# Optimization experiments

Measured on AMD Instinct MI355X. Metric: run time of the kernel, lower is better.

## Reference

```python
import jax, jax.numpy as jnp
import numpy as np
import math

N = 50000      # nodes per type
E = 800000     # edges per relation
IN = 256
OUT = 256
H = 8
DK = OUT // H  # 32
SQRT_DK = math.sqrt(DK)


def setup_inputs() -> dict:
    key = jax.random.key(0)
    ks = jax.random.split(key, 24)
    s = 0.02
    inp = {
        'h_A': jax.random.normal(ks[0], (N, IN), jnp.float32),
        'h_B': jax.random.normal(ks[1], (N, IN), jnp.float32),
        'src0': jax.random.randint(ks[2], (E,), 0, N, jnp.int32),
        'dst0': jax.random.randint(ks[3], (E,), 0, N, jnp.int32),
        'src1': jax.random.randint(ks[4], (E,), 0, N, jnp.int32),
        'dst1': jax.random.randint(ks[5], (E,), 0, N, jnp.int32),
        'src2': jax.random.randint(ks[6], (E,), 0, N, jnp.int32),
        'dst2': jax.random.randint(ks[7], (E,), 0, N, jnp.int32),
        # per-node-type linears (2 types): y = x @ W + b
        'Wk': jax.random.normal(ks[8], (2, IN, OUT), jnp.float32) * s,
        'bk': jnp.zeros((2, OUT), jnp.float32),
        'Wq': jax.random.normal(ks[9], (2, IN, OUT), jnp.float32) * s,
        'bq': jnp.zeros((2, OUT), jnp.float32),
        'Wv': jax.random.normal(ks[10], (2, IN, OUT), jnp.float32) * s,
        'bv': jnp.zeros((2, OUT), jnp.float32),
        'Wa': jax.random.normal(ks[11], (2, OUT, OUT), jnp.float32) * s,
        'ba': jnp.zeros((2, OUT), jnp.float32),
        # per-relation params (3 relations)
        'rel_att': jax.random.normal(ks[12], (3, H, DK, DK), jnp.float32) * (1.0 / math.sqrt(DK)),
        'rel_msg': jax.random.normal(ks[13], (3, H, DK, DK), jnp.float32) * (1.0 / math.sqrt(DK)),
        'rel_pri': jnp.ones((3, H), jnp.float32),
        'skip': jnp.ones((2,), jnp.float32),
    }
    return inp


def _relation_flow(k_src, v_src, q_dst, A_r, M_r, pri_r, src, dst):
    # k_src/v_src/q_dst: [N,H,DK] ; A_r,M_r: [H,DK,DK] ; pri_r: [H]
    k = jnp.einsum('bij,ijk->bik', k_src, A_r)
    v = jnp.einsum('bij,ijk->bik', v_src, M_r)
    # edge-wise dot: sum_d q[dst] * k[src] per head -> [E,H]
    score = jnp.einsum('ehd,ehd->eh', q_dst[dst], k[src]) * pri_r / SQRT_DK
    # edge softmax normalized by dst
    mx = jax.ops.segment_max(score, dst, num_segments=N)
    ex = jnp.exp(score - mx[dst])
    den = jax.ops.segment_sum(ex, dst, num_segments=N)
    attn = ex / den[dst]                       # [E,H]
    msg = v[src] * attn[:, :, None]            # [E,H,DK]
    return jax.ops.segment_sum(msg, dst, num_segments=N)  # [N,H,DK]


def reference(h_A, h_B, src0, dst0, src1, dst1, src2, dst2,
              Wk, bk, Wq, bq, Wv, bv, Wa, ba,
              rel_att, rel_msg, rel_pri, skip):
    h = [h_A, h_B]
    hd = lambda x: x.reshape(-1, H, DK)
    k = [hd(h[t] @ Wk[t] + bk[t]) for t in range(2)]
    q = [hd(h[t] @ Wq[t] + bq[t]) for t in range(2)]
    v = [hd(h[t] @ Wv[t] + bv[t]) for t in range(2)]

    # relations: r0: A->B, r1: B->A, r2: A->B
    t0 = _relation_flow(k[0], v[0], q[1], rel_att[0], rel_msg[0], rel_pri[0], src0, dst0)
    t1 = _relation_flow(k[1], v[1], q[0], rel_att[1], rel_msg[1], rel_pri[1], src1, dst1)
    t2 = _relation_flow(k[0], v[0], q[1], rel_att[2], rel_msg[2], rel_pri[2], src2, dst2)

    # cross_reducer='mean' over relations delivering to each dst type
    t_A = t1.reshape(N, OUT)
    t_B = ((t0 + t2) * 0.5).reshape(N, OUT)

    def out_for(tn, nid):
        alpha = jax.nn.sigmoid(skip[nid])
        trans = tn @ Wa[nid] + ba[nid]   # dropout is identity at eval
        return trans * alpha + h[nid] * (1.0 - alpha)

    new_h_A = out_for(t_A, 0)
    new_h_B = out_for(t_B, 1)
    return jnp.stack([new_h_A, new_h_B])  # [2, N, OUT]
```

## Files before the change

kernel.cpp:

```cpp
#include <hip/hip_runtime.h>
#include <math.h>

#define NN 50000
#define EE 800000
#define CC 256
#define NS (NN * CC)
#define NBK 782
#define BCAP 2048
#define P1T 2048
#define NT1 391

typedef __attribute__((ext_vector_type(4))) float f32x4;
typedef __attribute__((ext_vector_type(8))) short bf16x8;
typedef __attribute__((ext_vector_type(4))) unsigned int u32x4;
typedef __attribute__((ext_vector_type(2))) unsigned int u32x2;

__device__ __forceinline__ float bf2f(unsigned int u) {
    union { unsigned int i; float f; } c; c.i = u << 16; return c.f;
}
__device__ __forceinline__ unsigned short f2bf(float f) {
    union { float f; unsigned int i; } c; c.f = f;
    unsigned int u = c.i;
    u += 0x7fffu + ((u >> 16) & 1u);
    return (unsigned short)(u >> 16);
}

#if __has_builtin(__builtin_amdgcn_cvt_f32_fp8) && __has_builtin(__builtin_amdgcn_cvt_pk_fp8_f32)
#define HW_FP8 1
#else
#define HW_FP8 0
#endif

__device__ __forceinline__ unsigned char sw_f2fp8(float f) {
    float a = fabsf(f);
    unsigned s = (f < 0.f) ? 0x80u : 0u;
    if (a >= 448.f) return (unsigned char)(s | 0x7Eu);
    if (a < 0.015625f) {
        int q = (int)(a * 512.f + 0.5f);
        return (unsigned char)(s | (unsigned)q);
    }
    int e = (int)floorf(log2f(a));
    float m = ldexpf(a, -e);
    int q = (int)(m * 8.f + 0.5f);
    if (q == 16) { q = 8; e += 1; }
    if (e > 8) return (unsigned char)(s | 0x7Eu);
    return (unsigned char)(s | ((unsigned)(e + 7) << 3) | (unsigned)(q - 8));
}
__device__ __forceinline__ float sw_fp82f(unsigned b) {
    unsigned s = (b & 0x80u) << 24;
    unsigned exp = (b >> 3) & 0xFu, man = b & 7u;
    float val = (exp == 0) ? ldexpf((float)man, -9)
                           : ldexpf((float)(8u | man), (int)exp - 10);
    unsigned r = __builtin_bit_cast(unsigned, val) | s;
    return __builtin_bit_cast(float, r);
}
__device__ __forceinline__ unsigned char f2fp8(float f) {
#if HW_FP8
    return (unsigned char)(__builtin_amdgcn_cvt_pk_fp8_f32(f, 0.f, 0, false) & 0xff);
#else
    return sw_f2fp8(f);
#endif
}

__global__ void tobf_kernel(const float* __restrict__ hA, const float* __restrict__ hB,
                            unsigned short* __restrict__ h_bf)
{
    int id = blockIdx.x * 256 + threadIdx.x;
    if (id >= 2 * NS / 8) return;
    size_t base = (size_t)id * 8;
    const float* src = (base < (size_t)NS) ? (hA + base) : (hB + (base - NS));
    f32x4 a = *(const f32x4*)src;
    f32x4 b = *(const f32x4*)(src + 4);
    u32x4 o;
    o[0] = (unsigned)f2bf(a[0]) | ((unsigned)f2bf(a[1]) << 16);
    o[1] = (unsigned)f2bf(a[2]) | ((unsigned)f2bf(a[3]) << 16);
    o[2] = (unsigned)f2bf(b[0]) | ((unsigned)f2bf(b[1]) << 16);
    o[3] = (unsigned)f2bf(b[2]) | ((unsigned)f2bf(b[3]) << 16);
    *(u32x4*)(h_bf + base) = o;
}

__global__ void setup_kernel(const float* __restrict__ Wk, const float* __restrict__ bk,
                             const float* __restrict__ Wq, const float* __restrict__ bq,
                             const float* __restrict__ Wv, const float* __restrict__ bv,
                             const float* __restrict__ Wa,
                             const float* __restrict__ rel_att, const float* __restrict__ rel_msg,
                             unsigned short* __restrict__ WT, float* __restrict__ ball,
                             const int* __restrict__ d0, const int* __restrict__ d1,
                             const int* __restrict__ d2, int* __restrict__ bcnt)
{
    int b = blockIdx.x;
    const int ts[3] = {0, 1, 0};
    if (b >= 2568) {
        int bb = b - 2568;
        int r = bb / NT1, tile = bb - r * NT1;
        const int* dp = r == 0 ? d0 : (r == 1 ? d1 : d2);
        __shared__ int hist[NBK];
        for (int i = threadIdx.x; i < NBK; i += 256) hist[i] = 0;
        __syncthreads();
        int base = tile * P1T;
        int lim = base + P1T; if (lim > EE) lim = EE;
        for (int i = base + threadIdx.x; i < lim; i += 256)
            atomicAdd(&hist[dp[i] >> 6], 1);
        __syncthreads();
        for (int i = threadIdx.x; i < NBK; i += 256)
            if (hist[i]) atomicAdd(&bcnt[r * NBK + i], hist[i]);
        return;
    }
    int id = b * 256 + threadIdx.x;
    if (id < 2 * 65536) {
        int t = id >> 16, rem = id & 65535;
        int n = rem >> 8, k = rem & 255;
        WT[t * 65536 + n * 256 + k] = f2bf(Wq[t * 65536 + k * 256 + n]);
    } else if (id < 5 * 65536) {
        int id2 = id - 2 * 65536;
        int r = id2 >> 16, rem = id2 & 65535;
        int n = rem >> 8, k = rem & 255;
        int h = n >> 5, j = n & 31;
        const float* wkb = Wk + ts[r] * 65536 + k * 256 + h * 32;
        const float* ab  = rel_att + r * 8192 + h * 1024 + j;
        float s = 0.f;
        #pragma unroll 8
        for (int d = 0; d < 32; ++d) s += wkb[d] * ab[d * 32];
        WT[(2 + r) * 65536 + n * 256 + k] = f2bf(s);
    } else if (id < 8 * 65536) {
        int id2 = id - 5 * 65536;
        int r = id2 >> 16, rem = id2 & 65535;
        int n = rem >> 8, k = rem & 255;
        int h = n >> 5, j = n & 31;
        const float* wvb = Wv + ts[r] * 65536 + k * 256 + h * 32;
        const float* mb  = rel_msg + r * 8192 + h * 1024 + j;
        float s = 0.f;
        #pragma unroll 8
        for (int d = 0; d < 32; ++d) s += wvb[d] * mb[d * 32];
        WT[(5 + r) * 65536 + n * 256 + k] = f2bf(s);
    } else if (id < 10 * 65536) {
        int id2 = id - 8 * 65536;
        int t = id2 >> 16, rem = id2 & 65535;
        int n = rem >> 8, k = rem & 255;
        WT[(8 + t) * 65536 + n * 256 + k] = f2bf(Wa[t * 65536 + k * 256 + n]);
    } else if (id < 10 * 65536 + 2048) {
        int id2 = id - 10 * 65536;
        int z = id2 >> 8, c = id2 & 255;
        float v;
        if (z < 2) {
            v = bq[z * 256 + c];
        } else if (z < 5) {
            int r = z - 2, h = c >> 5, j = c & 31;
            const float* bkb = bk + ts[r] * 256 + h * 32;
            const float* ab  = rel_att + r * 8192 + h * 1024 + j;
            v = 0.f;
            for (int d = 0; d < 32; ++d) v += bkb[d] * ab[d * 32];
        } else {
            int r = z - 5, h = c >> 5, j = c & 31;
            const float* bvb = bv + ts[r] * 256 + h * 32;
            const float* mb  = rel_msg + r * 8192 + h * 1024 + j;
            v = 0.f;
            for (int d = 0; d < 32; ++d) v += bvb[d] * mb[d * 32];
        }
        ball[z * 256 + c] = v;
    }
}

__global__ __launch_bounds__(1024) void bscan_kernel(const int* __restrict__ bcnt,
                                                     int* __restrict__ bbase,
                                                     int* __restrict__ bcur)
{
    int r = blockIdx.x;
    int t = threadIdx.x, lane = t & 63, w = t >> 6;
    __shared__ int wsum[16];
    int x = (t < NBK) ? bcnt[r * NBK + t] : 0;
    int v = x;
    #pragma unroll
    for (int ofs = 1; ofs < 64; ofs <<= 1) {
        int y = __shfl_up(v, ofs);
        if (lane >= ofs) v += y;
    }
    if (lane == 63) wsum[w] = v;
    __syncthreads();
    if (t < 16) {
        int wv = wsum[t];
        #pragma unroll
        for (int ofs = 1; ofs < 16; ofs <<= 1) {
            int y = __shfl_up(wv, ofs);
            if (t >= ofs) wv += y;
        }
        wsum[t] = wv;
    }
    __syncthreads();
    int excl = (w > 0 ? wsum[w - 1] : 0) + v - x;
    if (t < NBK) { bbase[r * (NBK + 1) + t] = excl; bcur[r * NBK + t] = excl; }
    if (t == NBK - 1) bbase[r * (NBK + 1) + NBK] = excl + x;
}

__global__ __launch_bounds__(256) void p1_kernel(const int* __restrict__ s0, const int* __restrict__ s1,
                                                 const int* __restrict__ s2,
                                                 const int* __restrict__ d0, const int* __restrict__ d1,
                                                 const int* __restrict__ d2,
                                                 int* __restrict__ bcur, unsigned int* __restrict__ srcS)
{
    int bb = blockIdx.x;
    int r = bb / NT1, tile = bb - r * NT1;
    const int* sp = r == 0 ? s0 : (r == 1 ? s1 : s2);
    const int* dp = r == 0 ? d0 : (r == 1 ? d1 : d2);
    __shared__ int hist[NBK];
    __shared__ int lbase[NBK];
    for (int i = threadIdx.x; i < NBK; i += 256) hist[i] = 0;
    __syncthreads();
    int base = tile * P1T;
    int lim = base + P1T; if (lim > EE) lim = EE;
    for (int i = base + threadIdx.x; i < lim; i += 256)
        atomicAdd(&hist[dp[i] >> 6], 1);
    __syncthreads();
    for (int i = threadIdx.x; i < NBK; i += 256)
        lbase[i] = hist[i] ? atomicAdd(&bcur[r * NBK + i], hist[i]) : 0;
    __syncthreads();
    unsigned int* out = srcS + (size_t)r * EE;
    for (int i = base + threadIdx.x; i < lim; i += 256) {
        int dv = dp[i];
        int bk = dv >> 6;
        int pos = atomicAdd(&lbase[bk], 1);
        out[pos] = ((unsigned)sp[i] << 6) | (unsigned)(dv & 63);
    }
}

__global__ __launch_bounds__(256) void p2_kernel(const int* __restrict__ bbase,
                                                 unsigned int* __restrict__ srcS,
                                                 int* __restrict__ offs)
{
    int r = blockIdx.x / NBK, bk = blockIdx.x - r * NBK;
    int base = bbase[r * (NBK + 1) + bk];
    int n = bbase[r * (NBK + 1) + bk + 1] - base;
    unsigned int* seg = srcS + (size_t)r * EE + base;
    __shared__ unsigned int vals[BCAP];
    __shared__ unsigned int sorted[BCAP];
    __shared__ int hist[64], hcur[64];
    int t = threadIdx.x;
    if (t < 64) hist[t] = 0;
    __syncthreads();
    for (int i = t; i < n; i += 256) {
        unsigned int v = seg[i];
        vals[i] = v;
        atomicAdd(&hist[v & 63], 1);
    }
    __syncthreads();
    if (t < 64) {
        int x = hist[t], v = x;
        #pragma unroll
        for (int ofs = 1; ofs < 64; ofs <<= 1) {
            int y = __shfl_up(v, ofs);
            if (t >= ofs) v += y;
        }
        int excl = v - x;
        hcur[t] = excl;
        int d = bk * 64 + t;
        if (d < NN) offs[r * (NN + 1) + d] = base + excl;
    }
    if (bk == NBK - 1 && t == 64) offs[r * (NN + 1) + NN] = EE;
    __syncthreads();
    for (int i = t; i < n; i += 256) {
        unsigned int v = vals[i];
        int pos = atomicAdd(&hcur[v & 63], 1);
        sorted[pos] = v >> 6;
    }
    __syncthreads();
    for (int i = t; i < n; i += 256) seg[i] = sorted[i];
}

__device__ __forceinline__ void gemm_body(const unsigned short* __restrict__ A,
                                          const unsigned short* __restrict__ W,
                                          const float* __restrict__ bias,
                                          unsigned short* __restrict__ Obf,
                                          unsigned char* __restrict__ Of8,
                                          int mBase, int nBase)
{
    __shared__ __align__(16) unsigned short As[128 * 64];
    __shared__ __align__(16) unsigned short Bs[128 * 64];

    int tid = threadIdx.x;
    int lane = tid & 63, wid = tid >> 6;
    int warpM = wid >> 1, warpN = wid & 1;

    f32x4 acc[4][4];
    #pragma unroll
    for (int i = 0; i < 4; ++i)
        #pragma unroll
        for (int j = 0; j < 4; ++j) acc[i][j] = (f32x4){0.f, 0.f, 0.f, 0.f};

    for (int kt = 0; kt < 4; ++kt) {
        int k0 = kt * 64;
        __syncthreads();
        #pragma unroll
        for (int i = 0; i < 4; ++i) {
            int c = tid + i * 256;
            int row = c >> 3, cc = c & 7;
            int gr = mBase + row; if (gr > NN - 1) gr = NN - 1;
            u32x4 av = *(const u32x4*)(A + (size_t)gr * CC + k0 + cc * 8);
            int sb = row * 128 + ((cc * 16) ^ ((row & 7) << 4));
            *(u32x4*)((char*)As + sb) = av;
            u32x4 bv = *(const u32x4*)(W + (nBase + row) * 256 + k0 + cc * 8);
            *(u32x4*)((char*)Bs + sb) = bv;
        }
        __syncthreads();
        #pragma unroll
        for (int kk = 0; kk < 2; ++kk) {
            bf16x8 af[4], bfr[4];
            int kb = kk * 64 + (lane >> 4) * 16;
            #pragma unroll
            for (int mi = 0; mi < 4; ++mi) {
                int row = warpM * 64 + mi * 16 + (lane & 15);
                int sb = row * 128 + (kb ^ ((row & 7) << 4));
                af[mi] = *(const bf16x8*)((const char*)As + sb);
            }
            #pragma unroll
            for (int ni = 0; ni < 4; ++ni) {
                int row = warpN * 64 + ni * 16 + (lane & 15);
                int sb = row * 128 + (kb ^ ((row & 7) << 4));
                bfr[ni] = *(const bf16x8*)((const char*)Bs + sb);
            }
            #pragma unroll
            for (int mi = 0; mi < 4; ++mi)
                #pragma unroll
                for (int ni = 0; ni < 4; ++ni)
                    acc[mi][ni] = __builtin_amdgcn_mfma_f32_16x16x32_bf16(af[mi], bfr[ni], acc[mi][ni], 0, 0, 0);
        }
    }

    #pragma unroll
    for (int mi = 0; mi < 4; ++mi) {
        #pragma unroll
        for (int ni = 0; ni < 4; ++ni) {
            int col = nBase + warpN * 64 + ni * 16 + (lane & 15);
            int row0 = mBase + warpM * 64 + mi * 16 + (lane >> 4) * 4;
            float b = bias[col];
            #pragma unroll
            for (int j = 0; j < 4; ++j) {
                int row = row0 + j;
                if (row < NN) {
                    float val = acc[mi][ni][j] + b;
                    if (Of8) Of8[(size_t)row * 512 + col] = f2fp8(val);
                    else     Obf[(size_t)row * 256 + col] = f2bf(val);
                }
            }
        }
    }
}

__global__ __launch_bounds__(256, 2)
void gemm8_kernel(const unsigned short* __restrict__ h_bf,
                  const unsigned short* __restrict__ WT, const float* __restrict__ ball,
                  unsigned short* __restrict__ Qb, unsigned char* __restrict__ KV0,
                  unsigned char* __restrict__ KV1, unsigned char* __restrict__ KV2)
{
    int z = blockIdx.z;
    const unsigned short* A = (z == 1 || z == 3 || z == 6) ? (h_bf + (size_t)NS) : h_bf;
    unsigned short* Obf = nullptr;
    unsigned char* Of8 = nullptr;
    switch (z) {
        case 0: Obf = Qb;               break;
        case 1: Obf = Qb + (size_t)NS;  break;
        case 2: Of8 = KV0;              break;
        case 3: Of8 = KV1;              break;
        case 4: Of8 = KV2;              break;
        case 5: Of8 = KV0 + 256;        break;
        case 6: Of8 = KV1 + 256;        break;
        default: Of8 = KV2 + 256;       break;
    }
    gemm_body(A, WT + z * 65536, ball + z * 256, Obf, Of8,
              blockIdx.x * 128, blockIdx.y * 128);
}

__global__ __launch_bounds__(256, 2)
void out_gemm_kernel(const unsigned short* __restrict__ A0, const unsigned short* __restrict__ A1,
                     const unsigned short* __restrict__ W0, const unsigned short* __restrict__ W1,
                     const float* __restrict__ b0, const float* __restrict__ b1,
                     float* __restrict__ OutF,
                     const float* __restrict__ hA, const float* __restrict__ hB,
                     const float* __restrict__ skip)
{
    int z = blockIdx.z;
    const unsigned short* A = z ? A1 : A0;
    const unsigned short* W = z ? W1 : W0;
    const float* bias = z ? b1 : b0;
    int mBase = blockIdx.x * 128;
    int nBase = blockIdx.y * 128;

    __shared__ __align__(16) unsigned short As[128 * 64];
    __shared__ __align__(16) unsigned short Bs[128 * 64];

    int tid = threadIdx.x;
    int lane = tid & 63, wid = tid >> 6;
    int warpM = wid >> 1, warpN = wid & 1;

    f32x4 acc[4][4];
    #pragma unroll
    for (int i = 0; i < 4; ++i)
        #pragma unroll
        for (int j = 0; j < 4; ++j) acc[i][j] = (f32x4){0.f, 0.f, 0.f, 0.f};

    for (int kt = 0; kt < 4; ++kt) {
        int k0 = kt * 64;
        __syncthreads();
        #pragma unroll
        for (int i = 0; i < 4; ++i) {
            int c = tid + i * 256;
            int row = c >> 3, cc = c & 7;
            int gr = mBase + row; if (gr > NN - 1) gr = NN - 1;
            u32x4 av = *(const u32x4*)(A + (size_t)gr * CC + k0 + cc * 8);
            int sb = row * 128 + ((cc * 16) ^ ((row & 7) << 4));
            *(u32x4*)((char*)As + sb) = av;
            u32x4 bv = *(const u32x4*)(W + (nBase + row) * 256 + k0 + cc * 8);
            *(u32x4*)((char*)Bs + sb) = bv;
        }
        __syncthreads();
        #pragma unroll
        for (int kk = 0; kk < 2; ++kk) {
            bf16x8 af[4], bfr[4];
            int kb = kk * 64 + (lane >> 4) * 16;
            #pragma unroll
            for (int mi = 0; mi < 4; ++mi) {
                int row = warpM * 64 + mi * 16 + (lane & 15);
                int sb = row * 128 + (kb ^ ((row & 7) << 4));
                af[mi] = *(const bf16x8*)((const char*)As + sb);
            }
            #pragma unroll
            for (int ni = 0; ni < 4; ++ni) {
                int row = warpN * 64 + ni * 16 + (lane & 15);
                int sb = row * 128 + (kb ^ ((row & 7) << 4));
                bfr[ni] = *(const bf16x8*)((const char*)Bs + sb);
            }
            #pragma unroll
            for (int mi = 0; mi < 4; ++mi)
                #pragma unroll
                for (int ni = 0; ni < 4; ++ni)
                    acc[mi][ni] = __builtin_amdgcn_mfma_f32_16x16x32_bf16(af[mi], bfr[ni], acc[mi][ni], 0, 0, 0);
        }
    }

    float alpha = 1.f / (1.f + __expf(-skip[z]));
    const float* hres = z ? hB : hA;

    #pragma unroll
    for (int mi = 0; mi < 4; ++mi) {
        #pragma unroll
        for (int ni = 0; ni < 4; ++ni) {
            int col = nBase + warpN * 64 + ni * 16 + (lane & 15);
            int row0 = mBase + warpM * 64 + mi * 16 + (lane >> 4) * 4;
            float b = bias[col];
            #pragma unroll
            for (int j = 0; j < 4; ++j) {
                int row = row0 + j;
                if (row < NN) {
                    float val = acc[mi][ni][j] + b;
                    float hv = hres[(size_t)row * CC + col];
                    OutF[(size_t)z * NS + (size_t)row * CC + col] = val * alpha + hv * (1.f - alpha);
                }
            }
        }
    }
}

__device__ __forceinline__ float fp8sel(unsigned int w, int sel) {
#if HW_FP8
    switch (sel) {
        case 0: return __builtin_amdgcn_cvt_f32_fp8((int)w, 0);
        case 1: return __builtin_amdgcn_cvt_f32_fp8((int)w, 1);
        case 2: return __builtin_amdgcn_cvt_f32_fp8((int)w, 2);
        default: return __builtin_amdgcn_cvt_f32_fp8((int)w, 3);
    }
#else
    return sw_fp82f((w >> (sel * 8)) & 0xffu);
#endif
}

__global__ __launch_bounds__(256)
void agg_kernel(const unsigned short* __restrict__ Q,
                const unsigned char* __restrict__ KV,
                const int* __restrict__ off, const int* __restrict__ srcS,
                const float* __restrict__ pri,
                unsigned short* __restrict__ Tb, int mode)
{
    int wid = (blockIdx.x * 256 + threadIdx.x) >> 6;
    if (wid >= NN) return;
    int lane = threadIdx.x & 63;
    int h = lane >> 3;
    float ps = pri[h] * 0.17677669529663687f;

    u32x2 qv = *(const u32x2*)(Q + (size_t)wid * CC + lane * 4);
    float q0 = bf2f(qv[0] & 0xffffu), q1 = bf2f(qv[0] >> 16);
    float q2 = bf2f(qv[1] & 0xffffu), q3 = bf2f(qv[1] >> 16);

    int beg = off[wid], end = off[wid + 1];
    float l = 0.f;
    float a0 = 0.f, a1 = 0.f, a2 = 0.f, a3 = 0.f;
    int n = end - beg;
    if (n > 0) {
        int p0 = beg + lane;
        int idx = srcS[p0 < end ? p0 : end - 1];
        int s = __shfl(idx, 0);
        unsigned int kw = *(const unsigned int*)(KV + (size_t)s * 512 + lane * 4);
        unsigned int vw = *(const unsigned int*)(KV + (size_t)s * 512 + 256 + lane * 4);
        for (int j = 0; j < n; ++j) {
            unsigned int kc = kw, vc = vw;
            int jn = j + 1;
            if (jn < n) {
                if ((jn & 63) == 0) {
                    int p = beg + jn + lane;
                    idx = srcS[p < end ? p : end - 1];
                }
                int sn = __shfl(idx, jn & 63);
                kw = *(const unsigned int*)(KV + (size_t)sn * 512 + lane * 4);
                vw = *(const unsigned int*)(KV + (size_t)sn * 512 + 256 + lane * 4);
            }
            float d = q0 * fp8sel(kc, 0) + q1 * fp8sel(kc, 1)
                    + q2 * fp8sel(kc, 2) + q3 * fp8sel(kc, 3);
            d += __shfl_xor(d, 1);
            d += __shfl_xor(d, 2);
            d += __shfl_xor(d, 4);
            float pw = __expf(d * ps);
            l += pw;
            a0 += pw * fp8sel(vc, 0);
            a1 += pw * fp8sel(vc, 1);
            a2 += pw * fp8sel(vc, 2);
            a3 += pw * fp8sel(vc, 3);
        }
    }
    float inv = (l > 0.f) ? 1.f / l : 0.f;
    float r0 = a0 * inv, r1 = a1 * inv, r2 = a2 * inv, r3 = a3 * inv;
    unsigned short* out = Tb + (size_t)wid * CC + lane * 4;
    if (mode) {
        u32x2 prev = *(const u32x2*)out;
        r0 = (r0 + bf2f(prev[0] & 0xffffu)) * 0.5f;
        r1 = (r1 + bf2f(prev[0] >> 16)) * 0.5f;
        r2 = (r2 + bf2f(prev[1] & 0xffffu)) * 0.5f;
        r3 = (r3 + bf2f(prev[1] >> 16)) * 0.5f;
    }
    u32x2 o;
    o[0] = (unsigned)f2bf(r0) | ((unsigned)f2bf(r1) << 16);
    o[1] = (unsigned)f2bf(r2) | ((unsigned)f2bf(r3) << 16);
    *(u32x2*)out = o;
}

extern "C" void kernel_launch(void* const* d_in, const int* in_sizes, int n_in,
                              void* d_out, int out_size, void* d_ws, size_t ws_size,
                              hipStream_t stream)
{
    const float* hA = (const float*)d_in[0];
    const float* hB = (const float*)d_in[1];
    const int* src0 = (const int*)d_in[2];
    const int* dst0 = (const int*)d_in[3];
    const int* src1 = (const int*)d_in[4];
    const int* dst1 = (const int*)d_in[5];
    const int* src2 = (const int*)d_in[6];
    const int* dst2 = (const int*)d_in[7];
    const float* Wk = (const float*)d_in[8];
    const float* bk = (const float*)d_in[9];
    const float* Wq = (const float*)d_in[10];
    const float* bq = (const float*)d_in[11];
    const float* Wv = (const float*)d_in[12];
    const float* bv = (const float*)d_in[13];
    const float* Wa = (const float*)d_in[14];
    const float* ba = (const float*)d_in[15];
    const float* rel_att = (const float*)d_in[16];
    const float* rel_msg = (const float*)d_in[17];
    const float* rel_pri = (const float*)d_in[18];
    const float* skip = (const float*)d_in[19];

    char* w = (char*)d_ws;
    auto alloc = [&](size_t bytes) {
        char* p = w;
        w += (bytes + 255) & ~(size_t)255;
        return p;
    };
    unsigned short* WT  = (unsigned short*)alloc((size_t)10 * 65536 * 2);
    float* ball         = (float*)alloc((size_t)8 * 256 * 4);
    unsigned short* Qb  = (unsigned short*)alloc((size_t)2 * NS * 2);
    unsigned char* KV0  = (unsigned char*)alloc((size_t)NN * 512);
    unsigned short* Tb  = (unsigned short*)alloc((size_t)2 * NS * 2);
    int* offs           = (int*)alloc((size_t)3 * (NN + 1) * 4);
    int* srcS           = (int*)alloc((size_t)3 * EE * 4);
    int* bcnt           = (int*)alloc((size_t)3 * NBK * 4);
    int* bbase          = (int*)alloc((size_t)3 * (NBK + 1) * 4);
    int* bcur           = (int*)alloc((size_t)3 * NBK * 4);

    unsigned char* dob = (unsigned char*)d_out;
    unsigned char* KV1 = dob;
    unsigned char* KV2 = dob + (size_t)NN * 512;
    unsigned short* h_bf = (unsigned short*)(dob + (size_t)2 * NN * 512);

    (void)hipMemsetAsync(bcnt, 0, (size_t)3 * NBK * 4, stream);

    tobf_kernel<<<12500, 256, 0, stream>>>(hA, hB, h_bf);
    setup_kernel<<<2568 + 3 * NT1, 256, 0, stream>>>(Wk, bk, Wq, bq, Wv, bv, Wa,
                                                     rel_att, rel_msg, WT, ball,
                                                     dst0, dst1, dst2, bcnt);
    bscan_kernel<<<3, 1024, 0, stream>>>(bcnt, bbase, bcur);
    p1_kernel<<<3 * NT1, 256, 0, stream>>>(src0, src1, src2, dst0, dst1, dst2,
                                           bcur, (unsigned int*)srcS);
    p2_kernel<<<3 * NBK, 256, 0, stream>>>(bbase, (unsigned int*)srcS, offs);

    gemm8_kernel<<<dim3(391, 2, 8), 256, 0, stream>>>(h_bf, WT, ball,
                                                      Qb, KV0, KV1, KV2);

    agg_kernel<<<12500, 256, 0, stream>>>(Qb + NS, KV0, offs + 0 * (NN + 1),
                                          srcS + 0 * EE, rel_pri + 0, Tb + NS, 0);
    agg_kernel<<<12500, 256, 0, stream>>>(Qb, KV1, offs + 1 * (NN + 1),
                                          srcS + 1 * EE, rel_pri + 8, Tb, 0);
    agg_kernel<<<12500, 256, 0, stream>>>(Qb + NS, KV2, offs + 2 * (NN + 1),
                                          srcS + 2 * EE, rel_pri + 16, Tb + NS, 1);

    out_gemm_kernel<<<dim3(391, 2, 2), 256, 0, stream>>>(
        Tb, Tb + NS, WT + 8 * 65536, WT + 9 * 65536, ba, ba + 256,
        (float*)d_out, hA, hB, skip);
}
```

Before: 562.7 us.

## Fuse bf16 conversion into setup, merge three aggregation kernels, reorder GEMM block mapping

Folds the input-to-bf16 conversion into the setup kernel, which removes one launch. Merges the three per-relation aggregation launches into one kernel in which each B-node warp handles both A->B relations. That averages them in registers and skips the bf16 read-modify-write of the intermediate. The GEMM grid is flattened so the 16 (z, n-tile) blocks for one M tile run next to each other, to improve reuse of the A tile across weight matrices. The cost is uneven work per warp: B-node warps do twice the edges of A-node warps.

```diff
diff --git a/kernel.cpp b/kernel.cpp
--- a/kernel.cpp
+++ b/kernel.cpp
@@ -9,6 +9,8 @@
 #define BCAP 2048
 #define P1T 2048
 #define NT1 391
+#define TOBF_BLKS 12500
+#define PREP_BLKS 2568
 
 typedef __attribute__((ext_vector_type(4))) float f32x4;
 typedef __attribute__((ext_vector_type(8))) short bf16x8;
@@ -61,25 +63,22 @@
     return sw_f2fp8(f);
 #endif
 }
-
-__global__ void tobf_kernel(const float* __restrict__ hA, const float* __restrict__ hB,
-                            unsigned short* __restrict__ h_bf)
-{
-    int id = blockIdx.x * 256 + threadIdx.x;
-    if (id >= 2 * NS / 8) return;
-    size_t base = (size_t)id * 8;
-    const float* src = (base < (size_t)NS) ? (hA + base) : (hB + (base - NS));
-    f32x4 a = *(const f32x4*)src;
-    f32x4 b = *(const f32x4*)(src + 4);
-    u32x4 o;
-    o[0] = (unsigned)f2bf(a[0]) | ((unsigned)f2bf(a[1]) << 16);
-    o[1] = (unsigned)f2bf(a[2]) | ((unsigned)f2bf(a[3]) << 16);
-    o[2] = (unsigned)f2bf(b[0]) | ((unsigned)f2bf(b[1]) << 16);
-    o[3] = (unsigned)f2bf(b[2]) | ((unsigned)f2bf(b[3]) << 16);
-    *(u32x4*)(h_bf + base) = o;
-}
-
-__global__ void setup_kernel(const float* __restrict__ Wk, const float* __restrict__ bk,
+__device__ __forceinline__ float fp8sel(unsigned int w, int sel) {
+#if HW_FP8
+    switch (sel) {
+        case 0: return __builtin_amdgcn_cvt_f32_fp8((int)w, 0);
+        case 1: return __builtin_amdgcn_cvt_f32_fp8((int)w, 1);
+        case 2: return __builtin_amdgcn_cvt_f32_fp8((int)w, 2);
+        default: return __builtin_amdgcn_cvt_f32_fp8((int)w, 3);
+    }
+#else
+    return sw_fp82f((w >> (sel * 8)) & 0xffu);
+#endif
+}
+
+__global__ void setup_kernel(const float* __restrict__ hA, const float* __restrict__ hB,
+                             unsigned short* __restrict__ h_bf,
+                             const float* __restrict__ Wk, const float* __restrict__ bk,
                              const float* __restrict__ Wq, const float* __restrict__ bq,
                              const float* __restrict__ Wv, const float* __restrict__ bv,
                              const float* __restrict__ Wa,
@@ -90,8 +89,22 @@
 {
     int b = blockIdx.x;
     const int ts[3] = {0, 1, 0};
-    if (b >= 2568) {
-        int bb = b - 2568;
+    if (b < TOBF_BLKS) {
+        int id = b * 256 + threadIdx.x;
+        size_t base = (size_t)id * 8;
+        const float* src = (base < (size_t)NS) ? (hA + base) : (hB + (base - NS));
+        f32x4 a = *(const f32x4*)src;
+        f32x4 bb2 = *(const f32x4*)(src + 4);
+        u32x4 o;
+        o[0] = (unsigned)f2bf(a[0]) | ((unsigned)f2bf(a[1]) << 16);
+        o[1] = (unsigned)f2bf(a[2]) | ((unsigned)f2bf(a[3]) << 16);
+        o[2] = (unsigned)f2bf(bb2[0]) | ((unsigned)f2bf(bb2[1]) << 16);
+        o[3] = (unsigned)f2bf(bb2[2]) | ((unsigned)f2bf(bb2[3]) << 16);
+        *(u32x4*)(h_bf + base) = o;
+        return;
+    }
+    if (b >= TOBF_BLKS + PREP_BLKS) {
+        int bb = b - (TOBF_BLKS + PREP_BLKS);
         int r = bb / NT1, tile = bb - r * NT1;
         const int* dp = r == 0 ? d0 : (r == 1 ? d1 : d2);
         __shared__ int hist[NBK];
@@ -106,7 +119,7 @@
             if (hist[i]) atomicAdd(&bcnt[r * NBK + i], hist[i]);
         return;
     }
-    int id = b * 256 + threadIdx.x;
+    int id = (b - TOBF_BLKS) * 256 + threadIdx.x;
     if (id < 2 * 65536) {
         int t = id >> 16, rem = id & 65535;
         int n = rem >> 8, k = rem & 255;
@@ -351,7 +364,11 @@
                   unsigned short* __restrict__ Qb, unsigned char* __restrict__ KV0,
                   unsigned char* __restrict__ KV1, unsigned char* __restrict__ KV2)
 {
-    int z = blockIdx.z;
+    int bid = blockIdx.x;
+    int mtile = bid >> 4;
+    int rem = bid & 15;
+    int z = rem >> 1;
+    int ntile = rem & 1;
     const unsigned short* A = (z == 1 || z == 3 || z == 6) ? (h_bf + (size_t)NS) : h_bf;
     unsigned short* Obf = nullptr;
     unsigned char* Of8 = nullptr;
@@ -366,7 +383,7 @@
         default: Of8 = KV2 + 256;       break;
     }
     gemm_body(A, WT + z * 65536, ball + z * 256, Obf, Of8,
-              blockIdx.x * 128, blockIdx.y * 128);
+              mtile * 128, ntile * 128);
 }
 
 __global__ __launch_bounds__(256, 2)
@@ -459,37 +476,12 @@
     }
 }
 
-__device__ __forceinline__ float fp8sel(unsigned int w, int sel) {
-#if HW_FP8
-    switch (sel) {
-        case 0: return __builtin_amdgcn_cvt_f32_fp8((int)w, 0);
-        case 1: return __builtin_amdgcn_cvt_f32_fp8((int)w, 1);
-        case 2: return __builtin_amdgcn_cvt_f32_fp8((int)w, 2);
-        default: return __builtin_amdgcn_cvt_f32_fp8((int)w, 3);
-    }
-#else
-    return sw_fp82f((w >> (sel * 8)) & 0xffu);
-#endif
-}
-
-__global__ __launch_bounds__(256)
-void agg_kernel(const unsigned short* __restrict__ Q,
-                const unsigned char* __restrict__ KV,
-                const int* __restrict__ off, const int* __restrict__ srcS,
-                const float* __restrict__ pri,
-                unsigned short* __restrict__ Tb, int mode)
-{
-    int wid = (blockIdx.x * 256 + threadIdx.x) >> 6;
-    if (wid >= NN) return;
-    int lane = threadIdx.x & 63;
-    int h = lane >> 3;
-    float ps = pri[h] * 0.17677669529663687f;
-
-    u32x2 qv = *(const u32x2*)(Q + (size_t)wid * CC + lane * 4);
-    float q0 = bf2f(qv[0] & 0xffffu), q1 = bf2f(qv[0] >> 16);
-    float q2 = bf2f(qv[1] & 0xffffu), q3 = bf2f(qv[1] >> 16);
-
-    int beg = off[wid], end = off[wid + 1];
+__device__ __forceinline__ void agg_pass(const unsigned char* __restrict__ KV,
+                                         const int* __restrict__ srcS,
+                                         int beg, int end, int lane,
+                                         float q0, float q1, float q2, float q3, float ps,
+                                         float& o0, float& o1, float& o2, float& o3)
+{
     float l = 0.f;
     float a0 = 0.f, a1 = 0.f, a2 = 0.f, a3 = 0.f;
     int n = end - beg;
@@ -525,19 +517,53 @@
         }
     }
     float inv = (l > 0.f) ? 1.f / l : 0.f;
-    float r0 = a0 * inv, r1 = a1 * inv, r2 = a2 * inv, r3 = a3 * inv;
-    unsigned short* out = Tb + (size_t)wid * CC + lane * 4;
-    if (mode) {
-        u32x2 prev = *(const u32x2*)out;
-        r0 = (r0 + bf2f(prev[0] & 0xffffu)) * 0.5f;
-        r1 = (r1 + bf2f(prev[0] >> 16)) * 0.5f;
-        r2 = (r2 + bf2f(prev[1] & 0xffffu)) * 0.5f;
-        r3 = (r3 + bf2f(prev[1] >> 16)) * 0.5f;
-    }
-    u32x2 o;
-    o[0] = (unsigned)f2bf(r0) | ((unsigned)f2bf(r1) << 16);
-    o[1] = (unsigned)f2bf(r2) | ((unsigned)f2bf(r3) << 16);
-    *(u32x2*)out = o;
+    o0 = a0 * inv; o1 = a1 * inv; o2 = a2 * inv; o3 = a3 * inv;
+}
+
+__global__ __launch_bounds__(256)
+void agg_all_kernel(const unsigned short* __restrict__ Q0, const unsigned short* __restrict__ Q1,
+                    const unsigned char* __restrict__ KV0, const unsigned char* __restrict__ KV1,
+                    const unsigned char* __restrict__ KV2,
+                    const int* __restrict__ offs, const int* __restrict__ srcS,
+                    const float* __restrict__ rel_pri,
+                    unsigned short* __restrict__ TbA, unsigned short* __restrict__ TbB)
+{
+    int w = (blockIdx.x * 256 + threadIdx.x) >> 6;
+    int lane = threadIdx.x & 63;
+    int h = lane >> 3;
+    const float rs = 0.17677669529663687f;
+
+    if (w < NN) {
+        int d = w;
+        u32x2 qv = *(const u32x2*)(Q1 + (size_t)d * CC + lane * 4);
+        float q0 = bf2f(qv[0] & 0xffffu), q1 = bf2f(qv[0] >> 16);
+        float q2 = bf2f(qv[1] & 0xffffu), q3 = bf2f(qv[1] >> 16);
+        float x0, x1, x2, x3, y0, y1, y2, y3;
+        agg_pass(KV0, (const int*)srcS, offs[d], offs[d + 1], lane,
+                 q0, q1, q2, q3, rel_pri[h] * rs, x0, x1, x2, x3);
+        const int* off2 = offs + 2 * (NN + 1);
+        agg_pass(KV2, (const int*)srcS + 2 * EE, off2[d], off2[d + 1], lane,
+                 q0, q1, q2, q3, rel_pri[16 + h] * rs, y0, y1, y2, y3);
+        unsigned short* out = TbB + (size_t)d * CC + lane * 4;
+        u32x2 o;
+        o[0] = (unsigned)f2bf((x0 + y0) * 0.5f) | ((unsigned)f2bf((x1 + y1) * 0.5f) << 16);
+        o[1] = (unsigned)f2bf((x2 + y2) * 0.5f) | ((unsigned)f2bf((x3 + y3) * 0.5f) << 16);
+        *(u32x2*)out = o;
+    } else if (w < 2 * NN) {
+        int d = w - NN;
+        u32x2 qv = *(const u32x2*)(Q0 + (size_t)d * CC + lane * 4);
+        float q0 = bf2f(qv[0] & 0xffffu), q1 = bf2f(qv[0] >> 16);
+        float q2 = bf2f(qv[1] & 0xffffu), q3 = bf2f(qv[1] >> 16);
+        float x0, x1, x2, x3;
+        const int* off1 = offs + (NN + 1);
+        agg_pass(KV1, (const int*)srcS + EE, off1[d], off1[d + 1], lane,
+                 q0, q1, q2, q3, rel_pri[8 + h] * rs, x0, x1, x2, x3);
+        unsigned short* out = TbA + (size_t)d * CC + lane * 4;
+        u32x2 o;
+        o[0] = (unsigned)f2bf(x0) | ((unsigned)f2bf(x1) << 16);
+        o[1] = (unsigned)f2bf(x2) | ((unsigned)f2bf(x3) << 16);
+        *(u32x2*)out = o;
+    }
 }
 
 extern "C" void kernel_launch(void* const* d_in, const int* in_sizes, int n_in,
@@ -589,24 +615,18 @@
 
     (void)hipMemsetAsync(bcnt, 0, (size_t)3 * NBK * 4, stream);
 
-    tobf_kernel<<<12500, 256, 0, stream>>>(hA, hB, h_bf);
-    setup_kernel<<<2568 + 3 * NT1, 256, 0, stream>>>(Wk, bk, Wq, bq, Wv, bv, Wa,
-                                                     rel_att, rel_msg, WT, ball,
-                                                     dst0, dst1, dst2, bcnt);
+    setup_kernel<<<TOBF_BLKS + PREP_BLKS + 3 * NT1, 256, 0, stream>>>(
+        hA, hB, h_bf, Wk, bk, Wq, bq, Wv, bv, Wa,
+        rel_att, rel_msg, WT, ball, dst0, dst1, dst2, bcnt);
     bscan_kernel<<<3, 1024, 0, stream>>>(bcnt, bbase, bcur);
     p1_kernel<<<3 * NT1, 256, 0, stream>>>(src0, src1, src2, dst0, dst1, dst2,
                                            bcur, (unsigned int*)srcS);
     p2_kernel<<<3 * NBK, 256, 0, stream>>>(bbase, (unsigned int*)srcS, offs);
 
-    gemm8_kernel<<<dim3(391, 2, 8), 256, 0, stream>>>(h_bf, WT, ball,
-                                                      Qb, KV0, KV1, KV2);
-
-    agg_kernel<<<12500, 256, 0, stream>>>(Qb + NS, KV0, offs + 0 * (NN + 1),
-                                          srcS + 0 * EE, rel_pri + 0, Tb + NS, 0);
-    agg_kernel<<<12500, 256, 0, stream>>>(Qb, KV1, offs + 1 * (NN + 1),
-                                          srcS + 1 * EE, rel_pri + 8, Tb, 0);
-    agg_kernel<<<12500, 256, 0, stream>>>(Qb + NS, KV2, offs + 2 * (NN + 1),
-                                          srcS + 2 * EE, rel_pri + 16, Tb + NS, 1);
+    gemm8_kernel<<<391 * 16, 256, 0, stream>>>(h_bf, WT, ball, Qb, KV0, KV1, KV2);
+
+    agg_all_kernel<<<25000, 256, 0, stream>>>(Qb, Qb + NS, KV0, KV1, KV2,
+                                              offs, srcS, rel_pri, Tb, Tb + NS);
 
     out_gemm_kernel<<<dim3(391, 2, 2), 256, 0, stream>>>(
         Tb, Tb + NS, WT + 8 * 65536, WT + 9 * 65536, ba, ba + 256,
```

Measured after the change: 526.8 us. -6.4%, faster.
